# Kernel optimization log

Hardware: AMD Instinct MI355X
Metric: run time of the kernel (lower is better)

Reference implementation:

```python
import jax, jax.numpy as jnp
import numpy as np

BLK = 32
BIT = 8
BN_EPS = 1e-5


def _ste(x, xq):
    # straight-through estimator: forward = xq, backward = identity
    return x + jax.lax.stop_gradient(xq - x)


def bfp_quant_act(x, bit=BIT, blk=BLK):
    # Block floating point: shared exponent over blocks of `blk` channels
    # at each (n, h, w); mantissa quantized to `bit` bits (incl. sign).
    N, C, H, W = x.shape
    xb = x.reshape(N, C // blk, blk, H, W)
    maxabs = jnp.max(jnp.abs(xb), axis=2, keepdims=True)
    e = jnp.floor(jnp.log2(jnp.maximum(maxabs, 1e-12)))  # shared exponent
    scale = jnp.exp2(e + 1.0 - (bit - 1))
    qmax = 2.0 ** (bit - 1)
    q = jnp.clip(jnp.round(xb / scale), -qmax, qmax - 1.0)
    xq = (q * scale).reshape(N, C, H, W)
    return _ste(x, xq)


def dsconv_weight_quant(w, bit=BIT, blk=BLK):
    # DSConv VQK: per-block (blk input channels, per output channel, per
    # spatial tap) integer quantization with a float per-block scale (KDS).
    O, I, kh, kw = w.shape
    wb = w.reshape(O, I // blk, blk, kh, kw)
    qmax = 2.0 ** (bit - 1) - 1.0
    scale = jnp.maximum(jnp.max(jnp.abs(wb), axis=2, keepdims=True), 1e-12) / qmax
    q = jnp.clip(jnp.round(wb / scale), -qmax - 1.0, qmax)
    wq = (q * scale).reshape(O, I, kh, kw)
    return _ste(w, wq)


def conv2d(x, w, stride, padding):
    return jax.lax.conv_general_dilated(
        x, w, window_strides=(stride, stride),
        padding=[(padding, padding), (padding, padding)],
        dimension_numbers=('NCHW', 'OIHW', 'NCHW'))


def batchnorm(x, g, b, m, v):
    inv = g / jnp.sqrt(v + BN_EPS)
    return x * inv[None, :, None, None] + (b - m * inv)[None, :, None, None]


def setup_inputs() -> dict:
    key = jax.random.key(0)
    ks = jax.random.split(key, 12)
    N, Cin, Cout, H, W = 64, 128, 256, 56, 56
    inp = {
        'x':  jax.random.normal(ks[0], (N, Cin, H, W), jnp.float32),
        'w1': jax.random.normal(ks[1], (Cout, Cin, 3, 3), jnp.float32) * 0.05,
        'w2': jax.random.normal(ks[2], (Cout, Cout, 3, 3), jnp.float32) * 0.05,
        'ws': jax.random.normal(ks[3], (Cout, Cin, 1, 1), jnp.float32) * 0.05,
        'bn1_g': jnp.ones((Cout,), jnp.float32),
        'bn1_b': jnp.zeros((Cout,), jnp.float32),
        'bn1_m': jax.random.normal(ks[4], (Cout,), jnp.float32) * 0.1,
        'bn1_v': jax.random.uniform(ks[5], (Cout,), jnp.float32, 0.5, 1.5),
        'bn2_g': jnp.ones((Cout,), jnp.float32),
        'bn2_b': jnp.zeros((Cout,), jnp.float32),
        'bn2_m': jax.random.normal(ks[6], (Cout,), jnp.float32) * 0.1,
        'bn2_v': jax.random.uniform(ks[7], (Cout,), jnp.float32, 0.5, 1.5),
        'bns_g': jnp.ones((Cout,), jnp.float32),
        'bns_b': jnp.zeros((Cout,), jnp.float32),
        'bns_m': jax.random.normal(ks[8], (Cout,), jnp.float32) * 0.1,
        'bns_v': jax.random.uniform(ks[9], (Cout,), jnp.float32, 0.5, 1.5),
    }
    return inp


def reference(x, w1, w2, ws, bn1_g, bn1_b, bn1_m, bn1_v,
              bn2_g, bn2_b, bn2_m, bn2_v, bns_g, bns_b, bns_m, bns_v):
    stride = 2
    # conv1 (DSConv 3x3, stride 2) -> BN -> ReLU -> BFP activation quant
    out = conv2d(x, dsconv_weight_quant(w1), stride, 1)
    out = jax.nn.relu(batchnorm(out, bn1_g, bn1_b, bn1_m, bn1_v))
    out = bfp_quant_act(out)
    # conv2 (DSConv 3x3, stride 1) -> BN
    out = conv2d(out, dsconv_weight_quant(w2), 1, 1)
    out = batchnorm(out, bn2_g, bn2_b, bn2_m, bn2_v)
    # downsample shortcut: DSConv 1x1 stride 2 -> BN
    sc = conv2d(x, dsconv_weight_quant(ws), stride, 0)
    sc = batchnorm(sc, bns_g, bns_b, bns_m, bns_v)
    out = jax.nn.relu(out + sc)
    out = bfp_quant_act(out)  # activation2 (last=False)
    return out
```

## Files before the change

### kernel.cpp

```cpp
#include <hip/hip_runtime.h>
#include <stdint.h>

typedef unsigned short u16;
typedef __bf16 bf16x8 __attribute__((ext_vector_type(8)));
typedef float f32x4 __attribute__((ext_vector_type(4)));

#define NB    64
#define CIN   128
#define COUT  256
#define PIMG  960
#define PTOT  61440

static constexpr size_t XT4_BYTES = (size_t)64*PTOT*8*2;
static constexpr size_t A1C_BYTES = (size_t)32*PTOT*8*2;
static constexpr size_t BT1_BYTES = (size_t)2*144*128*8*2;
static constexpr size_t BT2_BYTES = (size_t)2*304*128*8*2;
static constexpr size_t OFF_XT4  = 0;
static constexpr size_t OFF_A1C  = OFF_XT4 + XT4_BYTES;
static constexpr size_t OFF_B1   = OFF_A1C + A1C_BYTES;
static constexpr size_t OFF_B2   = OFF_B1 + BT1_BYTES;
static constexpr size_t OFF_BETA = OFF_B2 + BT2_BYTES;

static __device__ __forceinline__ u16 f2bf(float f) {
  uint32_t u = __float_as_uint(f);
  u += 0x7fffu + ((u >> 16) & 1u);
  return (u16)(u >> 16);
}

typedef const __attribute__((address_space(1))) uint32_t* gas1;
typedef __attribute__((address_space(3))) uint32_t* las3;
static __device__ __forceinline__ void gl16(const void* g, void* l) {
  __builtin_amdgcn_global_load_lds((gas1)(uintptr_t)g,
                                   (las3)(uint32_t)(uintptr_t)l, 16, 0, 0);
}

static __device__ __forceinline__ void quant2(float v0, float v1, float& o0, float& o1) {
  float mx = fmaxf(v0, v1);
  mx = fmaxf(mx, __shfl_xor(mx, 1));
  mx = fmaxf(mx, __shfl_xor(mx, 2));
  mx = fmaxf(mx, __shfl_xor(mx, 4));
  mx = fmaxf(mx, __shfl_xor(mx, 8));
  mx = fmaxf(mx, 1e-12f);
  const int e = (int)(__float_as_uint(mx) >> 23) - 127;
  const float scale = __uint_as_float((uint32_t)(e + 121) << 23);
  const float invs  = __uint_as_float((uint32_t)(133 - e) << 23);
  o0 = fminf(rintf(v0 * invs), 127.f) * scale;
  o1 = fminf(rintf(v1 * invs), 127.f) * scale;
}

__global__ void k_zero(u16* __restrict__ base) {
  const int pl  = blockIdx.x;
  const int img = blockIdx.y;
  const int t   = threadIdx.x;
  int p;
  if (pl < 64) {
    const int s  = pl >> 4;
    const int cx = (s & 1) ? 28 : 0;
    const int cy = ((s >> 1) & 1) ? 28 : 0;
    if (t < 29)      p = t*32 + cx;
    else if (t < 58) p = cy*32 + (t - 29);
    else return;
  } else {
    if      (t < 30)  p = t*32;
    else if (t < 60)  p = (t - 30)*32 + 29;
    else if (t < 90)  p = (t - 60);
    else if (t < 120) p = 29*32 + (t - 90);
    else return;
  }
  f32x4 z = {0.f, 0.f, 0.f, 0.f};
  *(f32x4*)((char*)base + ((size_t)pl*PTOT + (size_t)img*960 + p)*16) = z;
}

__global__ void k_transpose(const float* __restrict__ x, u16* __restrict__ xt4) {
  __shared__ float s[32][33];
  const int ht = blockIdx.x, ct = blockIdx.y, n = blockIdx.z;
  const int t = threadIdx.x, tc = t >> 5, tw = t & 31;
  const float* src = x + ((size_t)(n*CIN + ct*32))*3136 + ht*32;
#pragma unroll
  for (int i = 0; i < 4; ++i)
    s[tc + i*8][tw] = src[(size_t)(tc + i*8)*3136 + tw];
  __syncthreads();
  if (t < 128) {
    const int hw_l = t & 31, cg = t >> 5;
    const int hw = ht*32 + hw_l;
    const int h = hw / 56, w = hw % 56;
    const int py = h + 1, px = w + 1;
    const int sub = (py & 1)*2 + (px & 1);
    const int p = (py >> 1)*32 + (px >> 1);
    union { u16 v[8]; uint4 u; } vv;
#pragma unroll
    for (int j = 0; j < 8; ++j) vv.v[j] = f2bf(s[cg*8 + j][hw_l]);
    *(uint4*)&xt4[(((size_t)(sub*16 + ct*4 + cg))*PTOT + (size_t)n*960 + p)*8]
        = vv.u;
  }
}

__global__ void k_prep(const float* __restrict__ w1, const float* __restrict__ w2,
                       const float* __restrict__ wsc,
                       const float* __restrict__ g1, const float* __restrict__ b1,
                       const float* __restrict__ m1, const float* __restrict__ v1,
                       const float* __restrict__ g2, const float* __restrict__ b2,
                       const float* __restrict__ m2, const float* __restrict__ v2,
                       const float* __restrict__ gs, const float* __restrict__ bs,
                       const float* __restrict__ ms, const float* __restrict__ vs,
                       u16* __restrict__ B1, u16* __restrict__ B2,
                       float* __restrict__ beta)
{
  const int id = blockIdx.x*256 + threadIdx.x;
  if (id < 9216) {
    const int o = id / 36, rem = id % 36, ib = rem / 9, t = rem % 9;
    const float inv = g1[o] / sqrtf(v1[o] + 1e-5f);
    const float* base = w1 + (size_t)(o*CIN + ib*32)*9 + t;
    float mx = 0.f;
#pragma unroll 8
    for (int jj = 0; jj < 32; ++jj) mx = fmaxf(mx, fabsf(base[jj*9]));
    const float scale = fmaxf(mx, 1e-12f) / 127.0f;
#pragma unroll 8
    for (int jj = 0; jj < 32; ++jj) {
      float q = rintf(base[jj*9] / scale);
      q = fminf(fmaxf(q, -128.f), 127.f);
      const int kc = t*16 + ib*4 + (jj >> 3);
      B1[(((size_t)(o >> 7)*144 + kc)*128 + (o & 127))*8 + (jj & 7)]
          = f2bf(q * scale * inv);
    }
  } else if (id < 27648) {
    const int id2 = id - 9216;
    const int o = id2 / 72, rem = id2 % 72, ib = rem / 9, t = rem % 9;
    const float inv = g2[o] / sqrtf(v2[o] + 1e-5f);
    const float* base = w2 + (size_t)(o*COUT + ib*32)*9 + t;
    float mx = 0.f;
#pragma unroll 8
    for (int jj = 0; jj < 32; ++jj) mx = fmaxf(mx, fabsf(base[jj*9]));
    const float scale = fmaxf(mx, 1e-12f) / 127.0f;
#pragma unroll 8
    for (int jj = 0; jj < 32; ++jj) {
      float q = rintf(base[jj*9] / scale);
      q = fminf(fmaxf(q, -128.f), 127.f);
      const int kc = t*32 + ib*4 + (jj >> 3);
      B2[(((size_t)(o >> 7)*304 + kc)*128 + (o & 127))*8 + (jj & 7)]
          = f2bf(q * scale * inv);
    }
  } else if (id < 28672) {
    const int id3 = id - 27648;
    const int o = id3 >> 2, ib = id3 & 3;
    const float inv = gs[o] / sqrtf(vs[o] + 1e-5f);
    const float* base = wsc + (size_t)o*CIN + ib*32;
    float mx = 0.f;
#pragma unroll 8
    for (int jj = 0; jj < 32; ++jj) mx = fmaxf(mx, fabsf(base[jj]));
    const float scale = fmaxf(mx, 1e-12f) / 127.0f;
#pragma unroll 8
    for (int jj = 0; jj < 32; ++jj) {
      float q = rintf(base[jj] / scale);
      q = fminf(fmaxf(q, -128.f), 127.f);
      const int kc = 288 + ib*4 + (jj >> 3);
      B2[(((size_t)(o >> 7)*304 + kc)*128 + (o & 127))*8 + (jj & 7)]
          = f2bf(q * scale * inv);
    }
  } else if (id < 29184) {
    const int id4 = id - 28672;
    const int which = id4 >> 8, o = id4 & 255;
    if (which == 0) {
      beta[o] = b1[o] - m1[o] * (g1[o] / sqrtf(v1[o] + 1e-5f));
    } else {
      beta[256 + o] = (b2[o] - m2[o] * (g2[o] / sqrtf(v2[o] + 1e-5f)))
                    + (bs[o] - ms[o] * (gs[o] / sqrtf(vs[o] + 1e-5f)));
    }
  }
}

template<int MODE>
__global__ __launch_bounds__(512, 2)
void gemm_k(const u16* __restrict__ Ag, const u16* __restrict__ Ag2,
            const u16* __restrict__ Bg, const float* __restrict__ beta,
            u16* __restrict__ a1c, float* __restrict__ of32)
{
  __shared__ __align__(16) u16 As3[3][8][256][8];
  __shared__ __align__(16) u16 Bs2[2][8][2][128][8];

  const int tid = threadIdx.x;
  const int wv  = tid >> 6;
  const int ln  = tid & 63;
  const int wr  = wv >> 2;
  const int wc  = wv & 3;

  const int b = blockIdx.x;
  const int mtile = (b & 7)*30 + (b >> 3);
  const int gp0 = mtile * 256;

  constexpr int NT  = (MODE == 0) ? 18 : 38;
  constexpr int NKC = (MODE == 0) ? 144 : 304;

  auto a_src = [&](int kc) -> const char* {
    if (MODE == 1 && kc >= 288) {
      const int g = kc - 288;
      return (const char*)Ag2 + ((size_t)(48 + g)*PTOT + gp0)*16;
    } else if (MODE == 0) {
      const int t = kc >> 4, g = kc & 15;
      const int dy = t/3, dx = t - dy*3;
      const int sub = (dy & 1)*2 + (dx & 1);
      return (const char*)Ag +
             ((size_t)(sub*16 + g)*PTOT + gp0 + (dy >> 1)*32 + (dx >> 1))*16;
    } else {
      const int t = kc >> 5, g = kc & 31;
      const int dy = t/3, dx = t - dy*3;
      return (const char*)Ag + ((size_t)g*PTOT + gp0 + dy*32 + dx)*16;
    }
  };

  auto issueA4 = [&](int kt2, int slot) {
    const char* s = a_src(kt2*8 + wv) + (size_t)ln*16;
    char* d = (char*)&As3[slot][wv][0][0];
#pragma unroll
    for (int q = 0; q < 4; ++q) gl16(s + q*1024, d + q*1024);
  };
  auto issueB4 = [&](int kt2, int slot) {
    const int kc = kt2*8 + wv;
    const char* s0 = (const char*)Bg + (size_t)kc*2048 + (size_t)ln*16;
    const char* s1 = s0 + (size_t)NKC*2048;
    char* d = (char*)&Bs2[slot][wv][0][0][0];
    gl16(s0,        d);
    gl16(s0 + 1024, d + 1024);
    gl16(s1,        d + 2048);
    gl16(s1 + 1024, d + 3072);
  };

  const int quad = ln >> 4, l15 = ln & 15;
  const u16* aP = &As3[0][quad][wr*128 + l15][0];
  const u16* bP[4];
#pragma unroll
  for (int ni = 0; ni < 4; ++ni) {
    const int n_ = wc*64 + ni*16 + l15;
    bP[ni] = &Bs2[0][quad][n_ >> 7][n_ & 127][0];
  }

  f32x4 acc[8][4];
#pragma unroll
  for (int i = 0; i < 8; ++i)
#pragma unroll
    for (int j2 = 0; j2 < 4; ++j2)
      acc[i][j2] = (f32x4){0.f, 0.f, 0.f, 0.f};

  issueA4(0, 0); issueB4(0, 0);
  issueA4(1, 1); issueB4(1, 1);

  int sl = 0;
  for (int kt = 0; kt < NT; ++kt) {
    const int bsl = kt & 1;
    if (kt + 1 < NT) asm volatile("s_waitcnt vmcnt(8)" ::: "memory");
    else             asm volatile("s_waitcnt vmcnt(0)" ::: "memory");
    asm volatile("s_barrier" ::: "memory");

    const u16* aB = aP + sl*16384;
    const bool pre = (kt + 2 < NT);
    int s2 = sl + 2; if (s2 >= 3) s2 -= 3;
    const char* asrc = nullptr; char* adst = nullptr;
    if (pre) {
      asrc = a_src((kt + 2)*8 + wv) + (size_t)ln*16;
      adst = (char*)&As3[s2][wv][0][0];
    }

    bf16x8 bv[4];
#pragma unroll
    for (int ph = 0; ph < 4; ++ph) {
      const int ks = ph >> 1, mh = ph & 1;
      bf16x8 av[4];
#pragma unroll
      for (int q = 0; q < 4; ++q)
        av[q] = *(const bf16x8*)(aB + ks*8192 + (mh*4 + q)*128);
      if (mh == 0) {
#pragma unroll
        for (int ni = 0; ni < 4; ++ni)
          bv[ni] = *(const bf16x8*)(bP[ni] + bsl*16384 + ks*8192);
      }
      if (pre) gl16(asrc + ph*1024, adst + ph*1024);
      asm volatile("s_barrier" ::: "memory");
      asm volatile("s_waitcnt lgkmcnt(0)" ::: "memory");
      if (ph == 3 && pre) issueB4(kt + 2, bsl);
      __builtin_amdgcn_s_setprio(1);
#pragma unroll
      for (int q = 0; q < 4; ++q)
#pragma unroll
        for (int ni = 0; ni < 4; ++ni)
          acc[mh*4 + q][ni] = __builtin_amdgcn_mfma_f32_16x16x32_bf16(
              av[q], bv[ni], acc[mh*4 + q][ni], 0, 0, 0);
      __builtin_amdgcn_s_setprio(0);
    }
    sl = (sl == 2) ? 0 : sl + 1;
  }

  const int cbase = wc*64;
  float bt[4];
#pragma unroll
  for (int ni = 0; ni < 4; ++ni) bt[ni] = beta[cbase + ni*16 + l15];

  const int gpw = gp0 + wr*128;
  const int n0  = gpw / 960;
  const int r0  = gpw % 960;

  if constexpr (MODE == 0) {
#pragma unroll
    for (int mi = 0; mi < 8; ++mi)
#pragma unroll
      for (int r = 0; r < 4; ++r) {
        const int lo  = r0 + mi*16 + quad*4 + r;
        const int loc = (lo >= 960) ? lo - 960 : lo;
        if (loc < 896 && (loc & 31) < 28) {
          const int gp = gpw + mi*16 + quad*4 + r;
          float v[4];
#pragma unroll
          for (int ni = 0; ni < 4; ++ni) v[ni] = fmaxf(acc[mi][ni][r] + bt[ni], 0.f);
#pragma unroll
          for (int g = 0; g < 2; ++g) {
            float o0, o1;
            quant2(v[2*g], v[2*g+1], o0, o1);
            const int c0 = cbase + (2*g)*16 + l15;
            const int c1 = c0 + 16;
            a1c[((size_t)(c0 >> 3)*PTOT + gp + 33)*8 + (c0 & 7)]
                = (u16)(__float_as_uint(o0) >> 16);
            a1c[((size_t)(c1 >> 3)*PTOT + gp + 33)*8 + (c1 & 7)]
                = (u16)(__float_as_uint(o1) >> 16);
          }
        }
      }
  } else {
#pragma unroll
    for (int mi = 0; mi < 8; ++mi) {
      float ov[4][4];
#pragma unroll
      for (int r = 0; r < 4; ++r) {
        float v[4];
#pragma unroll
        for (int ni = 0; ni < 4; ++ni)
          v[ni] = fmaxf(acc[mi][ni][r] + bt[ni], 0.f);
#pragma unroll
        for (int g = 0; g < 2; ++g)
          quant2(v[2*g], v[2*g+1], ov[2*g][r], ov[2*g+1][r]);
      }
      const int lo   = r0 + mi*16 + quad*4;
      const int nimg = (lo >= 960) ? n0 + 1 : n0;
      const int loc  = (lo >= 960) ? lo - 960 : lo;
      const int x0 = loc & 31, y = loc >> 5;
      if (x0 < 28 && loc < 896) {
#pragma unroll
        for (int ni = 0; ni < 4; ++ni) {
          const int c = cbase + ni*16 + l15;
          f32x4 val = { ov[ni][0], ov[ni][1], ov[ni][2], ov[ni][3] };
          *(f32x4*)(of32 + ((size_t)(nimg*COUT + c)*28 + y)*28 + x0) = val;
        }
      }
    }
  }
}

extern "C" void kernel_launch(void* const* d_in, const int* in_sizes, int n_in,
                              void* d_out, int out_size, void* d_ws, size_t ws_size,
                              hipStream_t stream)
{
  (void)in_sizes; (void)n_in; (void)out_size; (void)ws_size;
  const float* x   = (const float*)d_in[0];
  const float* w1  = (const float*)d_in[1];
  const float* w2  = (const float*)d_in[2];
  const float* wsc = (const float*)d_in[3];
  const float* g1 = (const float*)d_in[4];
  const float* b1 = (const float*)d_in[5];
  const float* m1 = (const float*)d_in[6];
  const float* v1 = (const float*)d_in[7];
  const float* g2 = (const float*)d_in[8];
  const float* b2 = (const float*)d_in[9];
  const float* m2 = (const float*)d_in[10];
  const float* v2 = (const float*)d_in[11];
  const float* gs = (const float*)d_in[12];
  const float* bs = (const float*)d_in[13];
  const float* ms = (const float*)d_in[14];
  const float* vs = (const float*)d_in[15];

  char* ws = (char*)d_ws;
  u16* xt4  = (u16*)(ws + OFF_XT4);
  u16* a1c  = (u16*)(ws + OFF_A1C);
  u16* B1   = (u16*)(ws + OFF_B1);
  u16* B2   = (u16*)(ws + OFF_B2);
  float* beta = (float*)(ws + OFF_BETA);

  k_zero<<<dim3(96, 64), 128, 0, stream>>>(xt4);
  k_transpose<<<dim3(98, 4, 64), 256, 0, stream>>>(x, xt4);
  k_prep<<<114, 256, 0, stream>>>(w1, w2, wsc, g1, b1, m1, v1,
                                  g2, b2, m2, v2, gs, bs, ms, vs,
                                  B1, B2, beta);
  gemm_k<0><<<240, 512, 0, stream>>>(xt4, nullptr, B1, beta, a1c, nullptr);
  gemm_k<1><<<240, 512, 0, stream>>>(a1c, xt4, B2, beta + 256, nullptr, (float*)d_out);
}
```

Measured before the change: 372.4 us.

## Load GEMM B operand straight to registers and drop per-phase barriers

The B (weight) tiles are no longer staged through shared memory. Each wave now loads its B fragments from global memory straight into a double-buffered register set, one k-tile ahead. This removes the Bs2 LDS buffer, the intra-tile barriers and the LDS reads for B, and the k-loop is unrolled by two to ping-pong the register buffers. The trade-off is redundant global/L2 traffic for B across waves that share a column and higher register pressure, and the vmcnt accounting now relies on the compiler's automatic waits for the register loads.

```diff
diff --git a/kernel.cpp b/kernel.cpp
--- a/kernel.cpp
+++ b/kernel.cpp
@@ -176,7 +176,6 @@
             u16* __restrict__ a1c, float* __restrict__ of32)
 {
   __shared__ __align__(16) u16 As3[3][8][256][8];
-  __shared__ __align__(16) u16 Bs2[2][8][2][128][8];
 
   const int tid = threadIdx.x;
   const int wv  = tid >> 6;
@@ -214,25 +213,24 @@
 #pragma unroll
     for (int q = 0; q < 4; ++q) gl16(s + q*1024, d + q*1024);
   };
-  auto issueB4 = [&](int kt2, int slot) {
-    const int kc = kt2*8 + wv;
-    const char* s0 = (const char*)Bg + (size_t)kc*2048 + (size_t)ln*16;
-    const char* s1 = s0 + (size_t)NKC*2048;
-    char* d = (char*)&Bs2[slot][wv][0][0][0];
-    gl16(s0,        d);
-    gl16(s0 + 1024, d + 1024);
-    gl16(s1,        d + 2048);
-    gl16(s1 + 1024, d + 3072);
-  };
 
   const int quad = ln >> 4, l15 = ln & 15;
   const u16* aP = &As3[0][quad][wr*128 + l15][0];
-  const u16* bP[4];
+
+  const char* bL[4];
 #pragma unroll
   for (int ni = 0; ni < 4; ++ni) {
     const int n_ = wc*64 + ni*16 + l15;
-    bP[ni] = &Bs2[0][quad][n_ >> 7][n_ & 127][0];
-  }
+    bL[ni] = (const char*)Bg + ((size_t)(n_ >> 7)*NKC + quad)*2048
+                             + (size_t)(n_ & 127)*16;
+  }
+  auto loadB = [&](int kt1, bf16x8 (&dst)[4][2]) {
+#pragma unroll
+    for (int ni = 0; ni < 4; ++ni)
+#pragma unroll
+      for (int ks = 0; ks < 2; ++ks)
+        dst[ni][ks] = *(const bf16x8*)(bL[ni] + (size_t)kt1*16384 + ks*8192);
+  };
 
   f32x4 acc[8][4];
 #pragma unroll
@@ -241,26 +239,16 @@
     for (int j2 = 0; j2 < 4; ++j2)
       acc[i][j2] = (f32x4){0.f, 0.f, 0.f, 0.f};
 
-  issueA4(0, 0); issueB4(0, 0);
-  issueA4(1, 1); issueB4(1, 1);
-
-  int sl = 0;
-  for (int kt = 0; kt < NT; ++kt) {
-    const int bsl = kt & 1;
-    if (kt + 1 < NT) asm volatile("s_waitcnt vmcnt(8)" ::: "memory");
-    else             asm volatile("s_waitcnt vmcnt(0)" ::: "memory");
+  bf16x8 bA[4][2], bB[4][2];
+
+  auto tile = [&](int kt, int sl, bf16x8 (&bc)[4][2], bf16x8 (&bn)[4][2]) {
+    if (kt < NT - 1) asm volatile("s_waitcnt vmcnt(12)" ::: "memory");
+    else             asm volatile("s_waitcnt vmcnt(8)"  ::: "memory");
     asm volatile("s_barrier" ::: "memory");
-
+    int s2 = sl + 2; if (s2 >= 3) s2 -= 3;
+    if (kt + 2 < NT) issueA4(kt + 2, s2);
+    if (kt + 1 < NT) loadB(kt + 1, bn);
     const u16* aB = aP + sl*16384;
-    const bool pre = (kt + 2 < NT);
-    int s2 = sl + 2; if (s2 >= 3) s2 -= 3;
-    const char* asrc = nullptr; char* adst = nullptr;
-    if (pre) {
-      asrc = a_src((kt + 2)*8 + wv) + (size_t)ln*16;
-      adst = (char*)&As3[s2][wv][0][0];
-    }
-
-    bf16x8 bv[4];
 #pragma unroll
     for (int ph = 0; ph < 4; ++ph) {
       const int ks = ph >> 1, mh = ph & 1;
@@ -268,25 +256,27 @@
 #pragma unroll
       for (int q = 0; q < 4; ++q)
         av[q] = *(const bf16x8*)(aB + ks*8192 + (mh*4 + q)*128);
-      if (mh == 0) {
-#pragma unroll
-        for (int ni = 0; ni < 4; ++ni)
-          bv[ni] = *(const bf16x8*)(bP[ni] + bsl*16384 + ks*8192);
-      }
-      if (pre) gl16(asrc + ph*1024, adst + ph*1024);
-      asm volatile("s_barrier" ::: "memory");
-      asm volatile("s_waitcnt lgkmcnt(0)" ::: "memory");
-      if (ph == 3 && pre) issueB4(kt + 2, bsl);
       __builtin_amdgcn_s_setprio(1);
 #pragma unroll
       for (int q = 0; q < 4; ++q)
 #pragma unroll
         for (int ni = 0; ni < 4; ++ni)
           acc[mh*4 + q][ni] = __builtin_amdgcn_mfma_f32_16x16x32_bf16(
-              av[q], bv[ni], acc[mh*4 + q][ni], 0, 0, 0);
+              av[q], bc[ni][ks], acc[mh*4 + q][ni], 0, 0, 0);
       __builtin_amdgcn_s_setprio(0);
     }
-    sl = (sl == 2) ? 0 : sl + 1;
+    asm volatile("s_waitcnt lgkmcnt(0)" ::: "memory");
+  };
+
+  issueA4(0, 0);
+  loadB(0, bA);
+  issueA4(1, 1);
+
+  int sl = 0;
+#pragma unroll 1
+  for (int k2 = 0; k2 < NT/2; ++k2) {
+    tile(2*k2,     sl, bA, bB);  sl = (sl == 2) ? 0 : sl + 1;
+    tile(2*k2 + 1, sl, bB, bA);  sl = (sl == 2) ? 0 : sl + 1;
   }
 
   const int cbase = wc*64;
```

Result: slower. 404.9 us (+8.7%).
